# Performance work log

Hardware: AMD Instinct MI355X
Metric: run time of the kernel (lower is better)

The kernel has to match this reference:

```python
import jax, jax.numpy as jnp
import numpy as np

B, L, H = 2, 2048, 1536
I, N, R, K = 3072, 16, 96, 4


def setup_inputs() -> dict:
    key = jax.random.key(0)
    ks = jax.random.split(key, 10)
    rn = lambda k, shape, s: jax.random.normal(k, shape, jnp.float32) * s
    return {
        "hidden_states": rn(ks[0], (B, L, H), 1.0),
        "W_in": rn(ks[1], (2 * I, H), 0.02),
        "conv_w": rn(ks[2], (I, K), 0.1),
        "conv_b": rn(ks[3], (I,), 0.1),
        "W_x": rn(ks[4], (R + 2 * N, I), 0.02),
        "W_dt": rn(ks[5], (I, R), 0.02),
        "dt_bias": rn(ks[6], (I,), 0.1),
        # vLLM's weight loader stores A = -exp(A_log); replicate that here
        "A": -jnp.exp(rn(ks[7], (I, N), 0.5)),
        "D": jnp.ones((I,), jnp.float32),
        "W_out": rn(ks[8], (H, I), 0.02),
    }


def reference(hidden_states, W_in, conv_w, conv_b, W_x, W_dt, dt_bias, A, D, W_out):
    b, l, _ = hidden_states.shape
    k = conv_w.shape[1]
    n = A.shape[1]
    r = W_dt.shape[1]

    # in_proj -> [B,L,2I], split into ssm input x and gate
    proj = jnp.einsum("blh,eh->ble", hidden_states, W_in)
    x, gate = jnp.split(proj, 2, axis=-1)  # each [B,L,I]

    # causal depthwise conv1d over L (pad K-1 on the left) + SiLU
    xp = jnp.pad(x, ((0, 0), (k - 1, 0), (0, 0)))
    conv = sum(xp[:, j : j + l, :] * conv_w[:, j] for j in range(k)) + conv_b
    x = jax.nn.silu(conv)  # [B,L,I]

    # x_proj -> dt (rank R), B, C (each N)
    ssm_p = jnp.einsum("bli,pi->blp", x, W_x)
    dt_in, Bm, Cm = jnp.split(ssm_p, [r, r + n], axis=-1)

    # dt_proj (skip_bias_add) then softplus(dt + bias) inside the scan math
    dt = jnp.einsum("blr,ir->bli", dt_in, W_dt)
    delta = jax.nn.softplus(dt + dt_bias)  # [B,L,I]

    # selective scan: s_t = exp(delta_t * A) * s_{t-1} + delta_t * x_t * B_t
    def step(state, inp):
        d_t, u_t, B_t, C_t = inp  # [B,I], [B,I], [B,N], [B,N]
        dA = jnp.exp(d_t[..., None] * A)  # [B,I,N]
        state = state * dA + (d_t * u_t)[..., None] * B_t[:, None, :]
        y = jnp.einsum("bin,bn->bi", state, C_t)
        return state, y

    init = jnp.zeros((b, x.shape[-1], n), jnp.float32)
    _, ys = jax.lax.scan(
        step,
        init,
        (
            delta.transpose(1, 0, 2),
            x.transpose(1, 0, 2),
            Bm.transpose(1, 0, 2),
            Cm.transpose(1, 0, 2),
        ),
    )
    y = ys.transpose(1, 0, 2) + x * D  # skip connection via D
    y = y * jax.nn.silu(gate)

    # out_proj -> [B,L,H]
    return jnp.einsum("bli,hi->blh", y, W_out)
```

## Files before the change

kernel.cpp:

```cpp
#include <hip/hip_runtime.h>

typedef __attribute__((ext_vector_type(8))) short bf16x8;
typedef __attribute__((ext_vector_type(4))) float f32x4;

#define CCH 32
#define TCH 64

__device__ __forceinline__ unsigned short f2b(float f) {
    unsigned u = __float_as_uint(f);
    return (unsigned short)((u + 0x7fffu + ((u >> 16) & 1u)) >> 16);
}
__device__ __forceinline__ float b2f(unsigned short h) {
    return __uint_as_float(((unsigned)h) << 16);
}
__device__ __forceinline__ float softplus_f(float z) {
    return (z > 15.f) ? z : __logf(1.f + __expf(z));
}
__device__ __forceinline__ float silu_f(float g) {
    return g / (1.f + __expf(-g));
}

__device__ __forceinline__ void gload16(const unsigned short* g, unsigned short* l) {
    __builtin_amdgcn_global_load_lds(
        (const __attribute__((address_space(1))) void*)g,
        (__attribute__((address_space(3))) void*)l, 16, 0, 0);
}

__global__ __launch_bounds__(256)
void cast_all(const float* __restrict__ h, const float* __restrict__ win,
              const float* __restrict__ wx, const float* __restrict__ wdt,
              const float* __restrict__ wout,
              unsigned short* __restrict__ dh, unsigned short* __restrict__ dwin,
              unsigned short* __restrict__ dwx, unsigned short* __restrict__ dwdt,
              unsigned short* __restrict__ dwout) {
    const int n0 = 1572864, n1 = n0 + 2359296, n2 = n1 + 98304,
              n3 = n2 + 73728, n4 = n3 + 1179648;
    int i = blockIdx.x * 256 + threadIdx.x;
    const float* s; unsigned short* d; int off;
    if (i < n0)      { s = h;    d = dh;    off = i; }
    else if (i < n1) { s = win;  d = dwin;  off = i - n0; }
    else if (i < n2) { s = wx;   d = dwx;   off = i - n1; }
    else if (i < n3) { s = wdt;  d = dwdt;  off = i - n2; }
    else if (i < n4) { s = wout; d = dwout; off = i - n3; }
    else return;
    float4 v = reinterpret_cast<const float4*>(s)[off];
    ushort4 o;
    o.x = f2b(v.x); o.y = f2b(v.y); o.z = f2b(v.z); o.w = f2b(v.w);
    reinterpret_cast<ushort4*>(d)[off] = o;
}

template <int OP>
__global__ __launch_bounds__(256)
void gemm_mfma(const unsigned short* __restrict__ A, const unsigned short* __restrict__ W,
               void* __restrict__ Cout, int Kc, int lda, int ldw, int ldc,
               const float* __restrict__ bias, int silu_col0, long long czs) {
    __shared__ unsigned short As[2][128 * 32];
    __shared__ unsigned short Bs[2][128 * 32];
    const int tid = threadIdx.x;
    const int bm = blockIdx.y * 128;
    const int bn = blockIdx.x * 128;
    const int kz = blockIdx.z;
    A += (size_t)kz * Kc;
    W += (size_t)kz * Kc;
    const int lane = tid & 63;
    const int wave = tid >> 6;
    const int r_a = lane >> 2;
    const int k8 = (lane & 3) * 8;

    const unsigned short* gA0 = A + (size_t)(bm + wave * 16 + r_a) * lda + k8;
    const unsigned short* gA1 = A + (size_t)(bm + 64 + wave * 16 + r_a) * lda + k8;
    const unsigned short* gB0 = W + (size_t)(bn + wave * 16 + r_a) * ldw + k8;
    const unsigned short* gB1 = W + (size_t)(bn + 64 + wave * 16 + r_a) * ldw + k8;

    const int wm = (wave & 1) * 64;
    const int wn = (wave >> 1) * 64;
    const int lr = lane & 15;
    const int quad = lane >> 4;

    f32x4 acc[4][4];
    const f32x4 zero = {0.f, 0.f, 0.f, 0.f};
#pragma unroll
    for (int i = 0; i < 4; i++)
#pragma unroll
        for (int j = 0; j < 4; j++) acc[i][j] = zero;

    const int niter = Kc >> 5;
    gload16(gA0, As[0] + wave * 512);
    gload16(gA1, As[0] + (wave + 4) * 512);
    gload16(gB0, Bs[0] + wave * 512);
    gload16(gB1, Bs[0] + (wave + 4) * 512);

    for (int k = 0; k < niter; k++) {
        __syncthreads();
        if (k + 1 < niter) {
            const int off = (k + 1) << 5;
            const int nb = (k + 1) & 1;
            gload16(gA0 + off, As[nb] + wave * 512);
            gload16(gA1 + off, As[nb] + (wave + 4) * 512);
            gload16(gB0 + off, Bs[nb] + wave * 512);
            gload16(gB1 + off, Bs[nb] + (wave + 4) * 512);
        }
        const unsigned short* as = As[k & 1];
        const unsigned short* bs = Bs[k & 1];
        bf16x8 fa[4], fb[4];
#pragma unroll
        for (int mi = 0; mi < 4; mi++)
            fa[mi] = *reinterpret_cast<const bf16x8*>(as + (wm + mi * 16 + lr) * 32 + quad * 8);
#pragma unroll
        for (int ni = 0; ni < 4; ni++)
            fb[ni] = *reinterpret_cast<const bf16x8*>(bs + (wn + ni * 16 + lr) * 32 + quad * 8);
#pragma unroll
        for (int mi = 0; mi < 4; mi++)
#pragma unroll
            for (int ni = 0; ni < 4; ni++)
                acc[mi][ni] = __builtin_amdgcn_mfma_f32_16x16x32_bf16(fa[mi], fb[ni], acc[mi][ni], 0, 0, 0);
    }

#pragma unroll
    for (int mi = 0; mi < 4; mi++)
#pragma unroll
        for (int reg = 0; reg < 4; reg++) {
            int row = bm + wm + mi * 16 + quad * 4 + reg;
#pragma unroll
            for (int ni = 0; ni < 4; ni++) {
                int col = bn + wn + ni * 16 + lr;
                float v = acc[mi][ni][reg];
                if (OP == 0) {
                    float* Cf = (float*)Cout + (size_t)kz * czs;
                    Cf[(size_t)row * ldc + col] = v;
                } else if (OP == 2) {
                    if (col >= silu_col0) v = silu_f(v);
                    ((unsigned short*)Cout)[(size_t)row * ldc + col] = f2b(v);
                } else if (OP == 3) {
                    ((unsigned short*)Cout)[(size_t)row * ldc + col] = f2b(softplus_f(v + bias[col]));
                } else {
                    atomicAdd((float*)Cout + (size_t)row * ldc + col, v);
                }
            }
        }
}

__global__ __launch_bounds__(256)
void reduce_xpart(const float* __restrict__ xpart, float* __restrict__ ssmp,
                  unsigned short* __restrict__ dtin) {
    const int BL = 4096;
    int idx = blockIdx.x * 256 + threadIdx.x;
    int row = idx >> 5;
    int c4 = (idx & 31) * 4;
    float4 s = {0.f, 0.f, 0.f, 0.f};
#pragma unroll
    for (int z = 0; z < 8; z++) {
        float4 v = *reinterpret_cast<const float4*>(xpart + (size_t)z * BL * 128 + (size_t)row * 128 + c4);
        s.x += v.x; s.y += v.y; s.z += v.z; s.w += v.w;
    }
    *reinterpret_cast<float4*>(ssmp + (size_t)row * 128 + c4) = s;
    if (c4 < 96) {
        ushort4 o;
        o.x = f2b(s.x); o.y = f2b(s.y); o.z = f2b(s.z); o.w = f2b(s.w);
        *reinterpret_cast<ushort4*>(dtin + (size_t)row * 96 + c4) = o;
    }
}

__global__ __launch_bounds__(256)
void conv_silu8(const unsigned short* __restrict__ projbf, const float* __restrict__ cw,
                const float* __restrict__ cb, unsigned short* __restrict__ xc) {
    const int I = 3072, L = 2048, LD = 6144;
    int idx = blockIdx.x * 256 + threadIdx.x;
    int i8 = (idx % (I / 8)) * 8;
    int bl = idx / (I / 8);
    int l = bl & (L - 1);
    float s[8];
    {
        float4 b0 = *reinterpret_cast<const float4*>(cb + i8);
        float4 b1 = *reinterpret_cast<const float4*>(cb + i8 + 4);
        s[0]=b0.x; s[1]=b0.y; s[2]=b0.z; s[3]=b0.w; s[4]=b1.x; s[5]=b1.y; s[6]=b1.z; s[7]=b1.w;
    }
    float w[8][4];
#pragma unroll
    for (int c = 0; c < 8; c++) {
        float4 wr = *reinterpret_cast<const float4*>(cw + (i8 + c) * 4);
        w[c][0]=wr.x; w[c][1]=wr.y; w[c][2]=wr.z; w[c][3]=wr.w;
    }
#pragma unroll
    for (int j = 0; j < 4; j++) {
        if (l + j - 3 >= 0) {
            uint4 r = *reinterpret_cast<const uint4*>(projbf + (size_t)(bl + j - 3) * LD + i8);
            float xv[8];
            xv[0]=b2f((unsigned short)(r.x & 0xffff)); xv[1]=b2f((unsigned short)(r.x >> 16));
            xv[2]=b2f((unsigned short)(r.y & 0xffff)); xv[3]=b2f((unsigned short)(r.y >> 16));
            xv[4]=b2f((unsigned short)(r.z & 0xffff)); xv[5]=b2f((unsigned short)(r.z >> 16));
            xv[6]=b2f((unsigned short)(r.w & 0xffff)); xv[7]=b2f((unsigned short)(r.w >> 16));
#pragma unroll
            for (int c = 0; c < 8; c++) s[c] = fmaf(xv[c], w[c][j], s[c]);
        }
    }
    unsigned short o[8];
#pragma unroll
    for (int c = 0; c < 8; c++) o[c] = f2b(silu_f(s[c]));
    uint4 packed;
    packed.x = (unsigned)o[0] | ((unsigned)o[1] << 16);
    packed.y = (unsigned)o[2] | ((unsigned)o[3] << 16);
    packed.z = (unsigned)o[4] | ((unsigned)o[5] << 16);
    packed.w = (unsigned)o[6] | ((unsigned)o[7] << 16);
    *reinterpret_cast<uint4*>(xc + (size_t)bl * I + i8) = packed;
}

__global__ __launch_bounds__(256)
void scan_passA(const unsigned short* __restrict__ delta_bf, const unsigned short* __restrict__ xc,
                const float* __restrict__ ssmp, const float* __restrict__ Aw,
                float* __restrict__ S_local, float* __restrict__ sumDelta) {
    const int I = 3072, L = 2048;
    __shared__ float bc[TCH][32];
    int g = blockIdx.x * 256 + threadIdx.x;
    int i = g % I;
    int bcid = g / I;
    int c = bcid % CCH;
    int b = bcid / CCH;
    size_t rowbase = (size_t)b * L + (size_t)c * TCH;
    for (int e = threadIdx.x; e < TCH * 8; e += 256) {
        int t = e >> 3, q = e & 7;
        float4 v = *reinterpret_cast<const float4*>(ssmp + (rowbase + t) * 128 + 96 + q * 4);
        *reinterpret_cast<float4*>(&bc[t][q * 4]) = v;
    }
    __syncthreads();

    float Arow[16];
#pragma unroll
    for (int n = 0; n < 16; n++) Arow[n] = Aw[i * 16 + n];
    float st[16];
#pragma unroll
    for (int n = 0; n < 16; n++) st[n] = 0.f;
    float sumD = 0.f;

    size_t rowI = rowbase * I + i;
    for (int t = 0; t < TCH; t++) {
        float delta = b2f(delta_bf[rowI]);
        float du = delta * b2f(xc[rowI]);
        sumD += delta;
        float4 b0 = *reinterpret_cast<const float4*>(&bc[t][0]);
        float4 b1 = *reinterpret_cast<const float4*>(&bc[t][4]);
        float4 b2 = *reinterpret_cast<const float4*>(&bc[t][8]);
        float4 b3 = *reinterpret_cast<const float4*>(&bc[t][12]);
        const float bv[16] = {b0.x,b0.y,b0.z,b0.w, b1.x,b1.y,b1.z,b1.w,
                              b2.x,b2.y,b2.z,b2.w, b3.x,b3.y,b3.z,b3.w};
#pragma unroll
        for (int n = 0; n < 16; n++)
            st[n] = fmaf(st[n], __expf(delta * Arow[n]), du * bv[n]);
        rowI += I;
    }
    size_t obase = (size_t)bcid * 16 * I + i;
#pragma unroll
    for (int n = 0; n < 16; n++) S_local[obase + (size_t)n * I] = st[n];
    sumDelta[(size_t)bcid * I + i] = sumD;
}

__global__ __launch_bounds__(256)
void scan_passB(const float* __restrict__ S_local, const float* __restrict__ sumDelta,
                const float* __restrict__ Aw, float* __restrict__ state_in) {
    const int I = 3072;
    int g = blockIdx.x * 256 + threadIdx.x;
    int i = g % I;
    int bn = g / I;
    int n = bn & 15;
    int b = bn >> 4;
    float a = Aw[i * 16 + n];
    float state = 0.f;
    for (int c = 0; c < CCH; c++) {
        int bcid = b * CCH + c;
        size_t idx = ((size_t)bcid * 16 + n) * I + i;
        state_in[idx] = state;
        state = fmaf(state, __expf(a * sumDelta[(size_t)bcid * I + i]), S_local[idx]);
    }
}

__global__ __launch_bounds__(256)
void scan_passC(const unsigned short* __restrict__ projbf,
                const unsigned short* __restrict__ xc,
                const float* __restrict__ ssmp, const unsigned short* __restrict__ delta_bf,
                const float* __restrict__ Aw, const float* __restrict__ Dw,
                const float* __restrict__ state_in, unsigned short* __restrict__ ybf) {
    const int I = 3072, L = 2048, LD = 6144;
    __shared__ float bc[TCH][32];
    int g = blockIdx.x * 256 + threadIdx.x;
    int i = g % I;
    int bcid = g / I;
    int c = bcid % CCH;
    int b = bcid / CCH;
    size_t rowbase = (size_t)b * L + (size_t)c * TCH;
    for (int e = threadIdx.x; e < TCH * 8; e += 256) {
        int t = e >> 3, q = e & 7;
        float4 v = *reinterpret_cast<const float4*>(ssmp + (rowbase + t) * 128 + 96 + q * 4);
        *reinterpret_cast<float4*>(&bc[t][q * 4]) = v;
    }
    __syncthreads();

    float Arow[16];
#pragma unroll
    for (int n = 0; n < 16; n++) Arow[n] = Aw[i * 16 + n];
    float Dv = Dw[i];
    float st[16];
    size_t sbase = (size_t)bcid * 16 * I + i;
#pragma unroll
    for (int n = 0; n < 16; n++) st[n] = state_in[sbase + (size_t)n * I];

    size_t rowI = rowbase * I + i;
    size_t rowG = rowbase * LD + I + i;
    for (int t = 0; t < TCH; t++) {
        float delta = b2f(delta_bf[rowI]);
        float u = b2f(xc[rowI]);
        float du = delta * u;
        float4 b0 = *reinterpret_cast<const float4*>(&bc[t][0]);
        float4 b1 = *reinterpret_cast<const float4*>(&bc[t][4]);
        float4 b2 = *reinterpret_cast<const float4*>(&bc[t][8]);
        float4 b3 = *reinterpret_cast<const float4*>(&bc[t][12]);
        float4 c0 = *reinterpret_cast<const float4*>(&bc[t][16]);
        float4 c1 = *reinterpret_cast<const float4*>(&bc[t][20]);
        float4 c2 = *reinterpret_cast<const float4*>(&bc[t][24]);
        float4 c3 = *reinterpret_cast<const float4*>(&bc[t][28]);
        const float bv[16] = {b0.x,b0.y,b0.z,b0.w, b1.x,b1.y,b1.z,b1.w,
                              b2.x,b2.y,b2.z,b2.w, b3.x,b3.y,b3.z,b3.w};
        const float cv[16] = {c0.x,c0.y,c0.z,c0.w, c1.x,c1.y,c1.z,c1.w,
                              c2.x,c2.y,c2.z,c2.w, c3.x,c3.y,c3.z,c3.w};
        float y = 0.f;
#pragma unroll
        for (int n = 0; n < 16; n++) {
            st[n] = fmaf(st[n], __expf(delta * Arow[n]), du * bv[n]);
            y = fmaf(st[n], cv[n], y);
        }
        y = fmaf(u, Dv, y);
        y *= b2f(projbf[rowG]);
        ybf[rowI] = f2b(y);
        rowI += I;
        rowG += LD;
    }
}

extern "C" void kernel_launch(void* const* d_in, const int* in_sizes, int n_in,
                              void* d_out, int out_size, void* d_ws, size_t ws_size,
                              hipStream_t stream) {
    const float* hidden  = (const float*)d_in[0];
    const float* W_in    = (const float*)d_in[1];
    const float* conv_w  = (const float*)d_in[2];
    const float* conv_b  = (const float*)d_in[3];
    const float* W_x     = (const float*)d_in[4];
    const float* W_dt    = (const float*)d_in[5];
    const float* dt_bias = (const float*)d_in[6];
    const float* Aw      = (const float*)d_in[7];
    const float* Dw      = (const float*)d_in[8];
    const float* W_out   = (const float*)d_in[9];
    float* out = (float*)d_out;

    constexpr int Bsz = 2, L = 2048, H = 1536, I = 3072, R = 96;
    constexpr int BL = Bsz * L;
    constexpr int TwoI = 2 * I;

    char* base = (char*)d_ws;
    unsigned short* proj_bf  = (unsigned short*)base; base += (size_t)BL * TwoI * 2;
    unsigned short* delta_bf = (unsigned short*)base; base += (size_t)BL * I * 2;
    unsigned short* xc_bf    = (unsigned short*)base; base += (size_t)BL * I * 2;
    unsigned short* y_bf     = (unsigned short*)base; base += (size_t)BL * I * 2;
    float* ssmp              = (float*)base;          base += (size_t)BL * 128 * 4;
    float* xpart             = (float*)base;          base += (size_t)8 * BL * 128 * 4;
    unsigned short* dtin_bf  = (unsigned short*)base; base += (size_t)BL * R * 2;
    unsigned short* wx_bf    = (unsigned short*)base; base += (size_t)128 * I * 2;
    unsigned short* wdt_bf   = (unsigned short*)base; base += (size_t)I * R * 2;
    unsigned short* wout_bf  = (unsigned short*)base; base += (size_t)H * I * 2;
    unsigned short* h_bf     = (unsigned short*)base; base += (size_t)BL * H * 2;
    unsigned short* win_bf   = (unsigned short*)base; base += (size_t)TwoI * H * 2;
    float* S_local  = (float*)h_bf;
    float* sumDelta = S_local + (size_t)Bsz * CCH * 16 * I;
    float* state_in = sumDelta + (size_t)Bsz * CCH * I;

    dim3 blk(256);

    hipMemsetAsync(out, 0, (size_t)BL * H * 4, stream);
    cast_all<<<(5283840 + 255) / 256, blk, 0, stream>>>(
        hidden, W_in, W_x, W_dt, W_out, h_bf, win_bf, wx_bf, wdt_bf, wout_bf);

    gemm_mfma<2><<<dim3(TwoI / 128, BL / 128, 1), blk, 0, stream>>>(
        h_bf, win_bf, proj_bf, H, H, H, TwoI, nullptr, I, 0);

    conv_silu8<<<BL * I / 8 / 256, blk, 0, stream>>>(proj_bf, conv_w, conv_b, xc_bf);

    gemm_mfma<0><<<dim3(1, BL / 128, 8), blk, 0, stream>>>(
        xc_bf, wx_bf, xpart, I / 8, I, I, 128, nullptr, 0, (long long)BL * 128);
    reduce_xpart<<<BL * 32 / 256, blk, 0, stream>>>(xpart, ssmp, dtin_bf);

    gemm_mfma<3><<<dim3(I / 128, BL / 128, 1), blk, 0, stream>>>(
        dtin_bf, wdt_bf, delta_bf, R, R, R, I, dt_bias, 0, 0);

    scan_passA<<<Bsz * I * CCH / 256, blk, 0, stream>>>(
        delta_bf, xc_bf, ssmp, Aw, S_local, sumDelta);
    scan_passB<<<Bsz * 16 * I / 256, blk, 0, stream>>>(
        S_local, sumDelta, Aw, state_in);
    scan_passC<<<Bsz * I * CCH / 256, blk, 0, stream>>>(
        proj_bf, xc_bf, ssmp, delta_bf, Aw, Dw, state_in, y_bf);

    gemm_mfma<4><<<dim3(H / 128, BL / 128, 2), blk, 0, stream>>>(
        y_bf, wout_bf, out, I / 2, I, I, H, nullptr, 0, 0);
}
```

Measured before the change: 496.8 us.

## Triple-buffer GEMM LDS loads with explicit vmcnt waits; split out_proj K four ways

```diff
diff --git a/kernel.cpp b/kernel.cpp
--- a/kernel.cpp
+++ b/kernel.cpp
@@ -54,8 +54,8 @@
 void gemm_mfma(const unsigned short* __restrict__ A, const unsigned short* __restrict__ W,
                void* __restrict__ Cout, int Kc, int lda, int ldw, int ldc,
                const float* __restrict__ bias, int silu_col0, long long czs) {
-    __shared__ unsigned short As[2][128 * 32];
-    __shared__ unsigned short Bs[2][128 * 32];
+    __shared__ unsigned short As[3][4096];
+    __shared__ unsigned short Bs[3][4096];
     const int tid = threadIdx.x;
     const int bm = blockIdx.y * 128;
     const int bn = blockIdx.x * 128;
@@ -84,24 +84,29 @@
 #pragma unroll
         for (int j = 0; j < 4; j++) acc[i][j] = zero;
 
+#define STAGE(koff, j) do { \
+        gload16(gA0 + (koff), As[j] + wave * 512); \
+        gload16(gA1 + (koff), As[j] + (wave + 4) * 512); \
+        gload16(gB0 + (koff), Bs[j] + wave * 512); \
+        gload16(gB1 + (koff), Bs[j] + (wave + 4) * 512); \
+    } while (0)
+
     const int niter = Kc >> 5;
-    gload16(gA0, As[0] + wave * 512);
-    gload16(gA1, As[0] + (wave + 4) * 512);
-    gload16(gB0, Bs[0] + wave * 512);
-    gload16(gB1, Bs[0] + (wave + 4) * 512);
-
+    STAGE(0, 0);
+    if (niter > 1) STAGE(32, 1);
+
+    int ib = 0;
     for (int k = 0; k < niter; k++) {
-        __syncthreads();
-        if (k + 1 < niter) {
-            const int off = (k + 1) << 5;
-            const int nb = (k + 1) & 1;
-            gload16(gA0 + off, As[nb] + wave * 512);
-            gload16(gA1 + off, As[nb] + (wave + 4) * 512);
-            gload16(gB0 + off, Bs[nb] + wave * 512);
-            gload16(gB1 + off, Bs[nb] + (wave + 4) * 512);
+        if (k + 1 < niter)
+            asm volatile("s_waitcnt vmcnt(4)\n\ts_barrier" ::: "memory");
+        else
+            asm volatile("s_waitcnt vmcnt(0)\n\ts_barrier" ::: "memory");
+        if (k + 2 < niter) {
+            int is_ = ib + 2; if (is_ >= 3) is_ -= 3;
+            STAGE((k + 2) << 5, is_);
         }
-        const unsigned short* as = As[k & 1];
-        const unsigned short* bs = Bs[k & 1];
+        const unsigned short* as = As[ib];
+        const unsigned short* bs = Bs[ib];
         bf16x8 fa[4], fb[4];
 #pragma unroll
         for (int mi = 0; mi < 4; mi++)
@@ -114,7 +119,9 @@
 #pragma unroll
             for (int ni = 0; ni < 4; ni++)
                 acc[mi][ni] = __builtin_amdgcn_mfma_f32_16x16x32_bf16(fa[mi], fb[ni], acc[mi][ni], 0, 0, 0);
-    }
+        ib = (ib == 2) ? 0 : ib + 1;
+    }
+#undef STAGE
 
 #pragma unroll
     for (int mi = 0; mi < 4; mi++)
@@ -396,6 +403,6 @@
     scan_passC<<<Bsz * I * CCH / 256, blk, 0, stream>>>(
         proj_bf, xc_bf, ssmp, delta_bf, Aw, Dw, state_in, y_bf);
 
-    gemm_mfma<4><<<dim3(H / 128, BL / 128, 2), blk, 0, stream>>>(
-        y_bf, wout_bf, out, I / 2, I, I, H, nullptr, 0, 0);
-}
+    gemm_mfma<4><<<dim3(H / 128, BL / 128, 4), blk, 0, stream>>>(
+        y_bf, wout_bf, out, I / 4, I, I, H, nullptr, 0, 0);
+}
```

Result: slower. 531.6 us (+7.0%).
